# Kernel tuning notes

Hardware: AMD Instinct MI355X
Metric: run time of the kernel (lower is better)

## Reference

```python
import jax, jax.numpy as jnp
import numpy as np

B, NQ, NK = 32, 1, 4096
Q_SIZE = K_SIZE = 512
H = 256


def setup_inputs() -> dict:
    key = jax.random.key(0)
    ks = jax.random.split(key, 6)
    return {
        "queries": jax.random.normal(ks[0], (B, NQ, Q_SIZE), jnp.float32),
        "keys": jax.random.normal(ks[1], (B, NK, K_SIZE), jnp.float32),
        "values": jax.random.normal(ks[2], (B, NK, 1), jnp.float32),
        "W_q": jax.random.normal(ks[3], (Q_SIZE, H), jnp.float32) / np.sqrt(Q_SIZE),
        "W_k": jax.random.normal(ks[4], (K_SIZE, H), jnp.float32) / np.sqrt(K_SIZE),
        "w_v": jax.random.normal(ks[5], (H,), jnp.float32) / np.sqrt(H),
    }


def reference(queries, keys, values, W_q, W_k, w_v):
    # Project queries and keys to hidden dim
    q = jnp.einsum("bqd,dh->bqh", queries, W_q)            # [B, NQ, H]
    k = jnp.einsum("bkd,dh->bkh", keys, W_k)               # [B, NK, H]
    # Broadcast-add + tanh: [B, NQ, NK, H]
    features = jnp.tanh(q[:, :, None, :] + k[:, None, :, :])
    # Reduce hidden dim with w_v -> scores [B, NQ, NK]
    scores = jnp.einsum("bqkh,h->bqk", features, w_v)
    attn = jax.nn.softmax(scores, axis=-1)                 # [B, NQ, NK]
    # Module squeezes n_q dim (==1) and trailing value dim (==1)
    return attn[:, 0, :] * values[:, :, 0]                 # [B, NK]
```

## Files before the change

### kernel.cpp

```cpp
#include <hip/hip_runtime.h>
#include <cstdint>
#include <cstddef>

#define NB 32
#define NKEYS 4096
#define DQ 512
#define HDIM 256

#define BM 64
#define BK 64
#define LDK 72

typedef __attribute__((ext_vector_type(8))) short bf16x8;
typedef __attribute__((ext_vector_type(4))) float f32x4;

__device__ __forceinline__ unsigned short f2bf(float f) {
    union { float f; unsigned u; } v; v.f = f;
    unsigned r = v.u + 0x7FFFu + ((v.u >> 16) & 1u);
    return (unsigned short)(r >> 16);
}

__device__ __forceinline__ float tanh_fast(float x) {
    float e = __expf(2.0f * x);
    return 1.0f - 2.0f / (e + 1.0f);
}

__global__ void k_prep_wkT(const float* __restrict__ Wk, unsigned short* __restrict__ WkT) {
    int idx = blockIdx.x * 256 + threadIdx.x;
    int d = idx >> 8, h = idx & 255;
    WkT[h * DQ + d] = f2bf(Wk[idx]);
}

__global__ void k_qproj(const float* __restrict__ q, const float* __restrict__ Wq,
                        float* __restrict__ qp) {
    __shared__ float qrow[DQ];
    __shared__ float part[512];
    const int b = blockIdx.x;
    const int tid = threadIdx.x;
    qrow[tid] = q[b * DQ + tid];
    __syncthreads();
    const int h = tid & 255;
    const int half = tid >> 8;
    float s = 0.f;
    const int d0 = half * 256;
    #pragma unroll 8
    for (int d = d0; d < d0 + 256; ++d)
        s += qrow[d] * Wq[d * HDIM + h];
    part[tid] = s;
    __syncthreads();
    if (tid < 256) qp[b * HDIM + tid] = part[tid] + part[tid + 256];
}

__global__ __launch_bounds__(256, 3) void k_scores(
        const float* __restrict__ keys, const unsigned short* __restrict__ WkT,
        const float* __restrict__ qp, const float* __restrict__ wv,
        float* __restrict__ scores) {
    __shared__ unsigned short As[BM * LDK];
    __shared__ unsigned short Bs[HDIM * LDK];
    __shared__ float s_rows[BM];

    const int tid = threadIdx.x;
    const int lane = tid & 63;
    const int wid = tid >> 6;
    const int row0 = blockIdx.x * BM;
    const int b = row0 >> 12;
    const int l15 = lane & 15;
    const int l4  = lane >> 4;

    f32x4 acc[4][4];
    #pragma unroll
    for (int i = 0; i < 4; ++i)
        #pragma unroll
        for (int j = 0; j < 4; ++j)
            acc[i][j] = (f32x4){0.f, 0.f, 0.f, 0.f};

    for (int kt = 0; kt < DQ; kt += BK) {
        #pragma unroll
        for (int i = 0; i < 4; ++i) {
            int idx = tid + i * 256;
            int row = idx >> 4, q4 = idx & 15;
            const float4 v = *reinterpret_cast<const float4*>(
                &keys[(size_t)(row0 + row) * DQ + kt + q4 * 4]);
            ushort4 h4;
            h4.x = f2bf(v.x); h4.y = f2bf(v.y); h4.z = f2bf(v.z); h4.w = f2bf(v.w);
            *reinterpret_cast<ushort4*>(&As[row * LDK + q4 * 4]) = h4;
        }
        #pragma unroll
        for (int i = 0; i < 8; ++i) {
            int idx = tid + i * 256;
            int col = idx >> 3, j = idx & 7;
            const uint4 v = *reinterpret_cast<const uint4*>(
                &WkT[(size_t)col * DQ + kt + j * 8]);
            *reinterpret_cast<uint4*>(&Bs[col * LDK + j * 8]) = v;
        }
        __syncthreads();
        #pragma unroll
        for (int kk = 0; kk < BK; kk += 32) {
            bf16x8 a[4], bb[4];
            const int kb = kk + l4 * 8;
            #pragma unroll
            for (int i = 0; i < 4; ++i)
                a[i] = *reinterpret_cast<const bf16x8*>(&As[(i * 16 + l15) * LDK + kb]);
            #pragma unroll
            for (int j = 0; j < 4; ++j)
                bb[j] = *reinterpret_cast<const bf16x8*>(&Bs[(wid * 64 + j * 16 + l15) * LDK + kb]);
            #pragma unroll
            for (int i = 0; i < 4; ++i)
                #pragma unroll
                for (int j = 0; j < 4; ++j)
                    acc[i][j] = __builtin_amdgcn_mfma_f32_16x16x32_bf16(
                        a[i], bb[j], acc[i][j], 0, 0, 0);
        }
        __syncthreads();
    }

    if (tid < BM) s_rows[tid] = 0.f;
    __syncthreads();

    float qv[4], wvv[4];
    #pragma unroll
    for (int j = 0; j < 4; ++j) {
        int col = wid * 64 + j * 16 + l15;
        qv[j]  = qp[b * HDIM + col];
        wvv[j] = wv[col];
    }
    #pragma unroll
    for (int i = 0; i < 4; ++i) {
        #pragma unroll
        for (int r = 0; r < 4; ++r) {
            float p = 0.f;
            #pragma unroll
            for (int j = 0; j < 4; ++j) {
                float x = acc[i][j][r] + qv[j];
                p += tanh_fast(x) * wvv[j];
            }
            p += __shfl_xor(p, 1);
            p += __shfl_xor(p, 2);
            p += __shfl_xor(p, 4);
            p += __shfl_xor(p, 8);
            if (l15 == 0)
                atomicAdd(&s_rows[i * 16 + l4 * 4 + r], p);
        }
    }
    __syncthreads();
    if (tid < BM) scores[row0 + tid] = s_rows[tid];
}

__global__ void k_softmax(const float* __restrict__ scores, const float* __restrict__ values,
                          float* __restrict__ out) {
    __shared__ float red[8];
    const int b = blockIdx.x, tid = threadIdx.x;
    const float* s = scores + b * NKEYS;
    float v[16];
    float m = -1e30f;
    #pragma unroll
    for (int i = 0; i < 16; ++i) { v[i] = s[tid + i * 256]; m = fmaxf(m, v[i]); }
    #pragma unroll
    for (int off = 1; off < 64; off <<= 1) m = fmaxf(m, __shfl_xor(m, off));
    const int wid = tid >> 6;
    if ((tid & 63) == 0) red[wid] = m;
    __syncthreads();
    m = fmaxf(fmaxf(red[0], red[1]), fmaxf(red[2], red[3]));
    float sum = 0.f;
    #pragma unroll
    for (int i = 0; i < 16; ++i) { v[i] = __expf(v[i] - m); sum += v[i]; }
    #pragma unroll
    for (int off = 1; off < 64; off <<= 1) sum += __shfl_xor(sum, off);
    if ((tid & 63) == 0) red[4 + wid] = sum;
    __syncthreads();
    sum = red[4] + red[5] + red[6] + red[7];
    const float inv = 1.0f / sum;
    #pragma unroll
    for (int i = 0; i < 16; ++i) {
        int n = tid + i * 256;
        out[b * NKEYS + n] = v[i] * inv * values[b * NKEYS + n];
    }
}

extern "C" void kernel_launch(void* const* d_in, const int* in_sizes, int n_in,
                              void* d_out, int out_size, void* d_ws, size_t ws_size,
                              hipStream_t stream) {
    const float* queries = (const float*)d_in[0];
    const float* keys    = (const float*)d_in[1];
    const float* values  = (const float*)d_in[2];
    const float* Wq      = (const float*)d_in[3];
    const float* Wk      = (const float*)d_in[4];
    const float* wv      = (const float*)d_in[5];
    float* out = (float*)d_out;

    char* ws = (char*)d_ws;
    float* scores        = (float*)ws;
    float* qp            = (float*)(ws + 131072 * 4);
    unsigned short* WkT  = (unsigned short*)(ws + 131072 * 4 + 8192 * 4);

    hipLaunchKernelGGL(k_prep_wkT, dim3(512), dim3(256), 0, stream, Wk, WkT);
    hipLaunchKernelGGL(k_qproj,    dim3(NB),  dim3(512), 0, stream, queries, Wq, qp);
    hipLaunchKernelGGL(k_scores,   dim3(NB * NKEYS / BM), dim3(256), 0, stream,
                       keys, WkT, qp, wv, scores);
    hipLaunchKernelGGL(k_softmax,  dim3(NB),  dim3(256), 0, stream, scores, values, out);
}
```

Baseline: 459.0 us.

## Double-buffer score GEMM with direct-to-LDS loads and swizzle, retune helper kernels

The scores kernel now double-buffers its LDS tiles. Keys are prefetched into registers and W_k^T is loaded straight into LDS with global_load_lds, so the loads for the next K-slice overlap the MFMA work on the current one. Padded LDS rows are replaced by an XOR swizzle to avoid bank conflicts, and occupancy drops to 2 blocks per CU to make room for the doubled LDS. The W_k transpose is tiled through shared memory for coalescing, q-projection is split across more blocks, and softmax uses 1024 threads per block; these changes add complexity and extra barriers.

```diff
diff --git a/kernel.cpp b/kernel.cpp
--- a/kernel.cpp
+++ b/kernel.cpp
@@ -9,10 +9,12 @@
 
 #define BM 64
 #define BK 64
-#define LDK 72
 
 typedef __attribute__((ext_vector_type(8))) short bf16x8;
 typedef __attribute__((ext_vector_type(4))) float f32x4;
+
+typedef __attribute__((address_space(1))) const unsigned int g_u32;
+typedef __attribute__((address_space(3))) unsigned int l_u32;
 
 __device__ __forceinline__ unsigned short f2bf(float f) {
     union { float f; unsigned u; } v; v.f = f;
@@ -25,47 +27,86 @@
     return 1.0f - 2.0f / (e + 1.0f);
 }
 
+__device__ __forceinline__ void gload_lds16(const void* g, void* l) {
+    __builtin_amdgcn_global_load_lds((g_u32*)g, (l_u32*)l, 16, 0, 0);
+}
+
 __global__ void k_prep_wkT(const float* __restrict__ Wk, unsigned short* __restrict__ WkT) {
-    int idx = blockIdx.x * 256 + threadIdx.x;
-    int d = idx >> 8, h = idx & 255;
-    WkT[h * DQ + d] = f2bf(Wk[idx]);
+    __shared__ unsigned short t[64][65];
+    const int tid = threadIdx.x;
+    const int dt = (blockIdx.x >> 2) << 6;
+    const int ht = (blockIdx.x & 3) << 6;
+    #pragma unroll
+    for (int i = 0; i < 16; ++i) {
+        int idx = tid + i * 256;
+        int d = idx >> 6, h = idx & 63;
+        t[d][h] = f2bf(Wk[(size_t)(dt + d) * HDIM + ht + h]);
+    }
+    __syncthreads();
+    #pragma unroll
+    for (int i = 0; i < 16; ++i) {
+        int idx = tid + i * 256;
+        int h = idx >> 6, d = idx & 63;
+        WkT[(size_t)(ht + h) * DQ + dt + d] = t[d][h];
+    }
 }
 
 __global__ void k_qproj(const float* __restrict__ q, const float* __restrict__ Wq,
                         float* __restrict__ qp) {
     __shared__ float qrow[DQ];
-    __shared__ float part[512];
-    const int b = blockIdx.x;
+    __shared__ float part[256];
+    const int blk = blockIdx.x;
+    const int b = blk >> 2, hq = blk & 3;
     const int tid = threadIdx.x;
-    qrow[tid] = q[b * DQ + tid];
-    __syncthreads();
-    const int h = tid & 255;
-    const int half = tid >> 8;
+    qrow[tid]       = q[b * DQ + tid];
+    qrow[tid + 256] = q[b * DQ + tid + 256];
+    __syncthreads();
+    const int h = (hq << 6) + (tid & 63);
+    const int d0 = (tid >> 6) << 7;
     float s = 0.f;
-    const int d0 = half * 256;
-    #pragma unroll 8
-    for (int d = d0; d < d0 + 256; ++d)
+    #pragma unroll 4
+    for (int d = d0; d < d0 + 128; ++d)
         s += qrow[d] * Wq[d * HDIM + h];
     part[tid] = s;
     __syncthreads();
-    if (tid < 256) qp[b * HDIM + tid] = part[tid] + part[tid + 256];
-}
-
-__global__ __launch_bounds__(256, 3) void k_scores(
+    if (tid < 64)
+        qp[b * HDIM + (hq << 6) + tid] =
+            part[tid] + part[tid + 64] + part[tid + 128] + part[tid + 192];
+}
+
+__global__ __launch_bounds__(256, 2) void k_scores(
         const float* __restrict__ keys, const unsigned short* __restrict__ WkT,
         const float* __restrict__ qp, const float* __restrict__ wv,
         float* __restrict__ scores) {
-    __shared__ unsigned short As[BM * LDK];
-    __shared__ unsigned short Bs[HDIM * LDK];
-    __shared__ float s_rows[BM];
-
-    const int tid = threadIdx.x;
+    __shared__ __align__(16) unsigned short As[2][BM * BK];
+    __shared__ __align__(16) unsigned short Bs[2][HDIM * BK];
+    float* s_rows = reinterpret_cast<float*>(&As[0][0]);
+
+    const int tid  = threadIdx.x;
     const int lane = tid & 63;
-    const int wid = tid >> 6;
+    const int wid  = tid >> 6;
     const int row0 = blockIdx.x * BM;
-    const int b = row0 >> 12;
-    const int l15 = lane & 15;
-    const int l4  = lane >> 4;
+    const int b    = row0 >> 12;
+    const int l15  = lane & 15;
+    const int l4   = lane >> 4;
+
+    const int ar  = tid >> 4;
+    const int ac4 = tid & 15;
+    const float* aptr[4];
+    int awoff[4];
+    #pragma unroll
+    for (int i = 0; i < 4; ++i) {
+        const int row = ar + i * 16;
+        aptr[i]  = keys + (size_t)(row0 + row) * DQ + ac4 * 4;
+        awoff[i] = row * 128 + (((ac4 >> 1) ^ (row & 7)) << 4) + (ac4 & 1) * 8;
+    }
+    const int bcol = wid * 64 + (lane >> 3);
+    const int bsw  = (lane & 7) ^ ((lane >> 3) & 7);
+    const unsigned short* bptr = WkT + (size_t)bcol * DQ + bsw * 8;
+
+    const int r7 = l15 & 7;
+    const int asl0 = (l4 ^ r7) << 4;
+    const int asl1 = ((4 + l4) ^ r7) << 4;
 
     f32x4 acc[4][4];
     #pragma unroll
@@ -74,36 +115,45 @@
         for (int j = 0; j < 4; ++j)
             acc[i][j] = (f32x4){0.f, 0.f, 0.f, 0.f};
 
-    for (int kt = 0; kt < DQ; kt += BK) {
+    float4 rA[4];
+
+    #pragma unroll
+    for (int i = 0; i < 4; ++i) rA[i] = *reinterpret_cast<const float4*>(aptr[i]);
+    #pragma unroll
+    for (int q = 0; q < 8; ++q)
+        gload_lds16(bptr + q * (8 * DQ), &Bs[0][(wid * 64 + q * 8) * BK]);
+    #pragma unroll
+    for (int i = 0; i < 4; ++i) {
+        ushort4 h4;
+        h4.x = f2bf(rA[i].x); h4.y = f2bf(rA[i].y); h4.z = f2bf(rA[i].z); h4.w = f2bf(rA[i].w);
+        *reinterpret_cast<ushort4*>(reinterpret_cast<char*>(&As[0][0]) + awoff[i]) = h4;
+    }
+    __syncthreads();
+
+    #pragma unroll
+    for (int kt = 0; kt < 8; ++kt) {
+        const int cur = kt & 1;
+        if (kt < 7) {
+            #pragma unroll
+            for (int i = 0; i < 4; ++i)
+                rA[i] = *reinterpret_cast<const float4*>(aptr[i] + (kt + 1) * BK);
+            #pragma unroll
+            for (int q = 0; q < 8; ++q)
+                gload_lds16(bptr + (kt + 1) * BK + q * (8 * DQ),
+                            &Bs[cur ^ 1][(wid * 64 + q * 8) * BK]);
+        }
+        const char* Ab = reinterpret_cast<const char*>(&As[cur][0]);
+        const char* Bb = reinterpret_cast<const char*>(&Bs[cur][0]);
         #pragma unroll
-        for (int i = 0; i < 4; ++i) {
-            int idx = tid + i * 256;
-            int row = idx >> 4, q4 = idx & 15;
-            const float4 v = *reinterpret_cast<const float4*>(
-                &keys[(size_t)(row0 + row) * DQ + kt + q4 * 4]);
-            ushort4 h4;
-            h4.x = f2bf(v.x); h4.y = f2bf(v.y); h4.z = f2bf(v.z); h4.w = f2bf(v.w);
-            *reinterpret_cast<ushort4*>(&As[row * LDK + q4 * 4]) = h4;
-        }
-        #pragma unroll
-        for (int i = 0; i < 8; ++i) {
-            int idx = tid + i * 256;
-            int col = idx >> 3, j = idx & 7;
-            const uint4 v = *reinterpret_cast<const uint4*>(
-                &WkT[(size_t)col * DQ + kt + j * 8]);
-            *reinterpret_cast<uint4*>(&Bs[col * LDK + j * 8]) = v;
-        }
-        __syncthreads();
-        #pragma unroll
-        for (int kk = 0; kk < BK; kk += 32) {
+        for (int kk = 0; kk < 2; ++kk) {
+            const int sl = kk ? asl1 : asl0;
             bf16x8 a[4], bb[4];
-            const int kb = kk + l4 * 8;
             #pragma unroll
             for (int i = 0; i < 4; ++i)
-                a[i] = *reinterpret_cast<const bf16x8*>(&As[(i * 16 + l15) * LDK + kb]);
+                a[i] = *reinterpret_cast<const bf16x8*>(Ab + (i * 16 + l15) * 128 + sl);
             #pragma unroll
             for (int j = 0; j < 4; ++j)
-                bb[j] = *reinterpret_cast<const bf16x8*>(&Bs[(wid * 64 + j * 16 + l15) * LDK + kb]);
+                bb[j] = *reinterpret_cast<const bf16x8*>(Bb + (wid * 64 + j * 16 + l15) * 128 + sl);
             #pragma unroll
             for (int i = 0; i < 4; ++i)
                 #pragma unroll
@@ -112,6 +162,17 @@
                         a[i], bb[j], acc[i][j], 0, 0, 0);
         }
         __syncthreads();
+        if (kt < 7) {
+            #pragma unroll
+            for (int i = 0; i < 4; ++i) {
+                ushort4 h4;
+                h4.x = f2bf(rA[i].x); h4.y = f2bf(rA[i].y);
+                h4.z = f2bf(rA[i].z); h4.w = f2bf(rA[i].w);
+                *reinterpret_cast<ushort4*>(
+                    reinterpret_cast<char*>(&As[cur ^ 1][0]) + awoff[i]) = h4;
+            }
+            __syncthreads();
+        }
     }
 
     if (tid < BM) s_rows[tid] = 0.f;
@@ -148,31 +209,35 @@
 
 __global__ void k_softmax(const float* __restrict__ scores, const float* __restrict__ values,
                           float* __restrict__ out) {
-    __shared__ float red[8];
+    __shared__ float red[32];
     const int b = blockIdx.x, tid = threadIdx.x;
     const float* s = scores + b * NKEYS;
-    float v[16];
+    float v[4];
     float m = -1e30f;
     #pragma unroll
-    for (int i = 0; i < 16; ++i) { v[i] = s[tid + i * 256]; m = fmaxf(m, v[i]); }
+    for (int i = 0; i < 4; ++i) { v[i] = s[tid + i * 1024]; m = fmaxf(m, v[i]); }
     #pragma unroll
     for (int off = 1; off < 64; off <<= 1) m = fmaxf(m, __shfl_xor(m, off));
-    const int wid = tid >> 6;
-    if ((tid & 63) == 0) red[wid] = m;
-    __syncthreads();
-    m = fmaxf(fmaxf(red[0], red[1]), fmaxf(red[2], red[3]));
+    const int w = tid >> 6;
+    if ((tid & 63) == 0) red[w] = m;
+    __syncthreads();
+    m = red[0];
+    #pragma unroll
+    for (int i = 1; i < 16; ++i) m = fmaxf(m, red[i]);
     float sum = 0.f;
     #pragma unroll
-    for (int i = 0; i < 16; ++i) { v[i] = __expf(v[i] - m); sum += v[i]; }
+    for (int i = 0; i < 4; ++i) { v[i] = __expf(v[i] - m); sum += v[i]; }
     #pragma unroll
     for (int off = 1; off < 64; off <<= 1) sum += __shfl_xor(sum, off);
-    if ((tid & 63) == 0) red[4 + wid] = sum;
-    __syncthreads();
-    sum = red[4] + red[5] + red[6] + red[7];
+    if ((tid & 63) == 0) red[16 + w] = sum;
+    __syncthreads();
+    sum = red[16];
+    #pragma unroll
+    for (int i = 1; i < 16; ++i) sum += red[16 + i];
     const float inv = 1.0f / sum;
     #pragma unroll
-    for (int i = 0; i < 16; ++i) {
-        int n = tid + i * 256;
+    for (int i = 0; i < 4; ++i) {
+        int n = tid + i * 1024;
         out[b * NKEYS + n] = v[i] * inv * values[b * NKEYS + n];
     }
 }
@@ -193,9 +258,9 @@
     float* qp            = (float*)(ws + 131072 * 4);
     unsigned short* WkT  = (unsigned short*)(ws + 131072 * 4 + 8192 * 4);
 
-    hipLaunchKernelGGL(k_prep_wkT, dim3(512), dim3(256), 0, stream, Wk, WkT);
-    hipLaunchKernelGGL(k_qproj,    dim3(NB),  dim3(512), 0, stream, queries, Wq, qp);
+    hipLaunchKernelGGL(k_prep_wkT, dim3(32),   dim3(256),  0, stream, Wk, WkT);
+    hipLaunchKernelGGL(k_qproj,    dim3(128),  dim3(256),  0, stream, queries, Wq, qp);
     hipLaunchKernelGGL(k_scores,   dim3(NB * NKEYS / BM), dim3(256), 0, stream,
                        keys, WkT, qp, wv, scores);
-    hipLaunchKernelGGL(k_softmax,  dim3(NB),  dim3(256), 0, stream, scores, values, out);
-}
+    hipLaunchKernelGGL(k_softmax,  dim3(NB),   dim3(1024), 0, stream, scores, values, out);
+}
```

Result: faster. 414.6 us (-9.7%).
